# Optimization experiments

Measured on AMD Instinct MI355X. Metric: run time of the kernel, lower is better.

Reference implementation:

```python
import jax, jax.numpy as jnp
import numpy as np
from jax import lax

B, CO, CI, KH, KW, H, W = 32, 128, 128, 3, 3, 56, 56
STRIDE = (1, 1)
PADDING = ((1, 1), (1, 1))


def setup_inputs() -> dict:
    key = jax.random.key(0)
    k1, k2, k3, k4 = jax.random.split(key, 4)
    inp = jax.random.normal(k1, (B, CI, H, W), dtype=jnp.float32)
    eps = jax.random.normal(k2, (B, CO, CI, KH, KW), dtype=jnp.float32)
    # reset_parameters: psi ~ U(-6, -5); mu ~ U(-stdv, stdv), stdv = 1/sqrt(CI*KH*KW)
    weight_psi = jax.random.uniform(k3, (CO, CI, KH, KW), dtype=jnp.float32,
                                    minval=-6.0, maxval=-5.0)
    stdv = 1.0 / np.sqrt(CI * KH * KW)
    weight_mu = jax.random.uniform(k4, (CO, CI, KH, KW), dtype=jnp.float32,
                                   minval=-stdv, maxval=stdv)
    return {"input": inp, "eps": eps, "weight_psi": weight_psi, "weight_mu": weight_mu}


def reference(input, eps, weight_psi, weight_mu):
    # mul_exp_add: per-sample weight = eps * exp(psi) + mu  -> [B, CO, CI, KH, KW]
    weight = eps * jnp.exp(weight_psi) + weight_mu

    # Per-example conv (torch does it via groups = bs trick); here vmap over batch.
    def conv_one(x, w):  # x: [CI,H,W], w: [CO,CI,KH,KW]
        return lax.conv_general_dilated(
            x[None], w, window_strides=STRIDE, padding=PADDING,
            dimension_numbers=("NCHW", "OIHW", "NCHW"))[0]

    out = jax.vmap(conv_one)(input, weight)  # [B, CO, H, W]
    return out
```

## Files before the change

### kernel.cpp

```cpp
#include <hip/hip_runtime.h>
#include <hip/hip_bf16.h>

#define CO    128
#define CI    128
#define NPIX  3136
#define PH    58
#define PPIX  3364
#define HPX   232
#define SROW  272

typedef __bf16 bf16x8 __attribute__((ext_vector_type(8)));
typedef float  f32x4  __attribute__((ext_vector_type(4)));

__global__ void prep_all(const float* __restrict__ in,
                         const float* __restrict__ eps,
                         const float* __restrict__ psi,
                         const float* __restrict__ mu,
                         __bf16* __restrict__ wt,
                         __bf16* __restrict__ it) {
  __shared__ __align__(16) __bf16 T[64][136];
  const int bx = blockIdx.x, tid = threadIdx.x;

  if (bx < 2048) {
    int idx = bx * 256 + tid;
    int ci = idx & 127;
    int co = (idx >> 7) & 127;
    const float* e  = eps + (size_t)idx * 9;
    const float* ps = psi + (size_t)(co * CI + ci) * 9;
    const float* m  = mu  + (size_t)(co * CI + ci) * 9;
    float v[9];
#pragma unroll
    for (int p = 0; p < 9; ++p) v[p] = e[p] * __expf(ps[p]) + m[p];
    int b = idx >> 14;
    __bf16* w = wt + ((size_t)b * 9 * CO + co) * CI + ci;
#pragma unroll
    for (int p = 0; p < 9; ++p) w[(size_t)p * CO * CI] = (__bf16)v[p];
  } else if (bx < 2504) {
    int cid = (bx - 2048) * 256 + tid;
    int pid = cid >> 4;
    int chunk = cid & 15;
    int b = pid / 228;
    int e = pid - b * 228;
    int ph, pw;
    if (e < 58)       { ph = 0;       pw = e; }
    else if (e < 116) { ph = 57;      pw = e - 58; }
    else if (e < 172) { ph = e - 115; pw = 0; }
    else              { ph = e - 171; pw = 57; }
    f32x4 z = {0.f, 0.f, 0.f, 0.f};
    *(f32x4*)&it[((size_t)b * PPIX + ph * PH + pw) * CI + chunk * 8] = z;
  } else {
    int tx = bx - 2504;
    int b  = tx / 49;
    int p0 = (tx - b * 49) * 64;
    const float* src = in + (size_t)b * CI * NPIX;
#pragma unroll
    for (int jj = 0; jj < 8; ++jj) {
      int c = jj * 256 + tid;
      int ci = c >> 4, xc = c & 15;
      float4 v = *(const float4*)(src + (size_t)ci * NPIX + p0 + xc * 4);
      T[xc * 4 + 0][ci] = (__bf16)v.x;
      T[xc * 4 + 1][ci] = (__bf16)v.y;
      T[xc * 4 + 2][ci] = (__bf16)v.z;
      T[xc * 4 + 3][ci] = (__bf16)v.w;
    }
    __syncthreads();
    __bf16* dstb = it + (size_t)b * PPIX * CI;
#pragma unroll
    for (int jj = 0; jj < 4; ++jj) {
      int c = jj * 256 + tid;
      int pl = c >> 4, xc = c & 15;
      int pix = p0 + pl;
      int oh = pix / 56, ow = pix - oh * 56;
      int ppix = (oh + 1) * PH + (ow + 1);
      *(f32x4*)&dstb[(size_t)ppix * CI + xc * 8] = *(const f32x4*)&T[pl][xc * 8];
    }
  }
}

__device__ __forceinline__ void loadB(const char* Bsh, const int* bbase, int tapb,
                                      bf16x8 bf[7]) {
#pragma unroll
  for (int nf = 0; nf < 7; ++nf)
    bf[nf] = *(const bf16x8*)&Bsh[bbase[nf] + tapb];
}

__device__ __forceinline__ void loadA(const __bf16* wtb, const int* ab, int s,
                                      bf16x8 af[4]) {
  const int p   = s >> 2;
  const int ci0 = (s & 3) << 5;
  const __bf16* ap = wtb + p * (CO * CI) + ci0;
#pragma unroll
  for (int mf = 0; mf < 4; ++mf)
    af[mf] = *(const bf16x8*)(ap + ab[mf]);
}

__device__ __forceinline__ void do_mfma(const bf16x8 af[4], const bf16x8 bf[7],
                                        f32x4 acc[4][7]) {
#pragma unroll
  for (int mf = 0; mf < 4; ++mf)
#pragma unroll
    for (int nf = 0; nf < 7; ++nf)
      acc[mf][nf] = __builtin_amdgcn_mfma_f32_16x16x32_bf16(
          af[mf], bf[nf], acc[mf][nf], 0, 0, 0);
}

#define TAPB(s) ((((s) >> 2) / 3) * PH + (((s) >> 2) % 3)) * SROW + (((s) & 3) << 6)

__global__ __launch_bounds__(128, 1) void bconv_gemm(
    const __bf16* __restrict__ wt,
    const __bf16* __restrict__ it,
    float* __restrict__ out) {
  __shared__ __align__(16) char Bsh[HPX * SROW];
  const int tid  = threadIdx.x;
  const int w    = tid >> 6;
  const int lane = tid & 63;
  const int quad = lane >> 4;
  const int l15  = lane & 15;

  const int lin = blockIdx.x;
  const int x   = lin & 7;
  const int j   = lin >> 3;
  const int bhi = j & 3;
  const int tile = j >> 2;
  const int b   = x + 8 * bhi;
  const int oh0 = tile * 2;

  const __bf16* hsrc = it + ((size_t)b * PPIX + oh0 * PH) * CI;
#pragma unroll
  for (int i = 0; i < 29; ++i) {
    int idx = i * 128 + tid;
    int px = idx >> 4, sub = idx & 15;
    f32x4 v = *(const f32x4*)(hsrc + (size_t)idx * 8);
    *(f32x4*)&Bsh[px * SROW + sub * 16] = v;
  }
  __syncthreads();

  int bbase[7];
#pragma unroll
  for (int nf = 0; nf < 7; ++nf) {
    int n = nf * 16 + l15;
    int r = (n >= 56) ? 1 : 0;
    bbase[nf] = (n + 2 * r) * SROW + quad * 16;
  }

  const int co0 = w * 64;
  const __bf16* wtb = wt + (size_t)b * 9 * CO * CI;
  int ab[4];
#pragma unroll
  for (int mf = 0; mf < 4; ++mf)
    ab[mf] = (co0 + mf * 16 + l15) * CI + quad * 8;

  f32x4 acc[4][7] = {};
  bf16x8 a0[4], a1[4], b0[7], b1[7];

  loadA(wtb, ab, 0, a0);
  loadB(Bsh, bbase, TAPB(0), b0);
#pragma unroll
  for (int s = 0; s < 34; s += 2) {
    loadA(wtb, ab, s + 1, a1);
    loadB(Bsh, bbase, TAPB(s + 1), b1);
    do_mfma(a0, b0, acc);
    loadA(wtb, ab, s + 2, a0);
    loadB(Bsh, bbase, TAPB(s + 2), b0);
    do_mfma(a1, b1, acc);
  }
  loadA(wtb, ab, 35, a1);
  loadB(Bsh, bbase, TAPB(35), b1);
  do_mfma(a0, b0, acc);
  do_mfma(a1, b1, acc);

  float* ob = out + (size_t)b * CO * NPIX + oh0 * 56;
#pragma unroll
  for (int mf = 0; mf < 4; ++mf) {
#pragma unroll
    for (int nf = 0; nf < 7; ++nf) {
#pragma unroll
      for (int r = 0; r < 4; ++r) {
        int co = co0 + mf * 16 + quad * 4 + r;
        ob[(size_t)co * NPIX + nf * 16 + l15] = acc[mf][nf][r];
      }
    }
  }
}

extern "C" void kernel_launch(void* const* d_in, const int* in_sizes, int n_in,
                              void* d_out, int out_size, void* d_ws, size_t ws_size,
                              hipStream_t stream) {
  const float* inp = (const float*)d_in[0];
  const float* eps = (const float*)d_in[1];
  const float* psi = (const float*)d_in[2];
  const float* mu  = (const float*)d_in[3];

  __bf16* wt = (__bf16*)d_ws;
  __bf16* it = (__bf16*)((char*)d_ws + 9437184);

  prep_all<<<4072, 256, 0, stream>>>(inp, eps, psi, mu, wt, it);
  bconv_gemm<<<896, 128, 0, stream>>>(wt, it, (float*)d_out);
}
```

Measured before the change: 166.7 us.

## Load conv input tile directly from global memory instead of staging in LDS

Removes the shared-memory staging of the padded input halo (about 63 KB) and its barrier in the GEMM kernel. B fragments are now read straight from the bf16 NHWC input in global memory, relying on L1/L2 for reuse across taps. Launch bounds are raised to allow two blocks per CU now that LDS use is zero. The trade-off is more global/cache traffic per MFMA, with B fetches taking global-load latency instead of LDS latency.

```diff
diff --git a/kernel.cpp b/kernel.cpp
--- a/kernel.cpp
+++ b/kernel.cpp
@@ -6,8 +6,6 @@
 #define NPIX  3136
 #define PH    58
 #define PPIX  3364
-#define HPX   232
-#define SROW  272
 
 typedef __bf16 bf16x8 __attribute__((ext_vector_type(8)));
 typedef float  f32x4  __attribute__((ext_vector_type(4)));
@@ -77,13 +75,6 @@
   }
 }
 
-__device__ __forceinline__ void loadB(const char* Bsh, const int* bbase, int tapb,
-                                      bf16x8 bf[7]) {
-#pragma unroll
-  for (int nf = 0; nf < 7; ++nf)
-    bf[nf] = *(const bf16x8*)&Bsh[bbase[nf] + tapb];
-}
-
 __device__ __forceinline__ void loadA(const __bf16* wtb, const int* ab, int s,
                                       bf16x8 af[4]) {
   const int p   = s >> 2;
@@ -92,6 +83,17 @@
 #pragma unroll
   for (int mf = 0; mf < 4; ++mf)
     af[mf] = *(const bf16x8*)(ap + ab[mf]);
+}
+
+__device__ __forceinline__ void loadB(const __bf16* itb, const int* br, int s,
+                                      bf16x8 bf[7]) {
+  const int p   = s >> 2;
+  const int ci0 = (s & 3) << 5;
+  const int kh  = p / 3, kw = p - kh * 3;
+  const int off = (kh * PH + kw - (PH + 1)) * CI + ci0;
+#pragma unroll
+  for (int nf = 0; nf < 7; ++nf)
+    bf[nf] = *(const bf16x8*)(itb + br[nf] + off);
 }
 
 __device__ __forceinline__ void do_mfma(const bf16x8 af[4], const bf16x8 bf[7],
@@ -104,13 +106,10 @@
           af[mf], bf[nf], acc[mf][nf], 0, 0, 0);
 }
 
-#define TAPB(s) ((((s) >> 2) / 3) * PH + (((s) >> 2) % 3)) * SROW + (((s) & 3) << 6)
-
-__global__ __launch_bounds__(128, 1) void bconv_gemm(
+__global__ __launch_bounds__(128, 2) void bconv_gemm(
     const __bf16* __restrict__ wt,
     const __bf16* __restrict__ it,
     float* __restrict__ out) {
-  __shared__ __align__(16) char Bsh[HPX * SROW];
   const int tid  = threadIdx.x;
   const int w    = tid >> 6;
   const int lane = tid & 63;
@@ -125,47 +124,40 @@
   const int b   = x + 8 * bhi;
   const int oh0 = tile * 2;
 
-  const __bf16* hsrc = it + ((size_t)b * PPIX + oh0 * PH) * CI;
-#pragma unroll
-  for (int i = 0; i < 29; ++i) {
-    int idx = i * 128 + tid;
-    int px = idx >> 4, sub = idx & 15;
-    f32x4 v = *(const f32x4*)(hsrc + (size_t)idx * 8);
-    *(f32x4*)&Bsh[px * SROW + sub * 16] = v;
-  }
-  __syncthreads();
-
-  int bbase[7];
-#pragma unroll
-  for (int nf = 0; nf < 7; ++nf) {
-    int n = nf * 16 + l15;
-    int r = (n >= 56) ? 1 : 0;
-    bbase[nf] = (n + 2 * r) * SROW + quad * 16;
-  }
+  const __bf16* wtb = wt + (size_t)b * 9 * CO * CI;
+  const __bf16* itb = it + (size_t)b * PPIX * CI;
 
   const int co0 = w * 64;
-  const __bf16* wtb = wt + (size_t)b * 9 * CO * CI;
   int ab[4];
 #pragma unroll
   for (int mf = 0; mf < 4; ++mf)
     ab[mf] = (co0 + mf * 16 + l15) * CI + quad * 8;
 
+  int br[7];
+#pragma unroll
+  for (int nf = 0; nf < 7; ++nf) {
+    int n = nf * 16 + l15;
+    int r = (n >= 56) ? 1 : 0;
+    int c = n - r * 56;
+    br[nf] = ((oh0 + 1 + r) * PH + (c + 1)) * CI + quad * 8;
+  }
+
   f32x4 acc[4][7] = {};
   bf16x8 a0[4], a1[4], b0[7], b1[7];
 
   loadA(wtb, ab, 0, a0);
-  loadB(Bsh, bbase, TAPB(0), b0);
+  loadB(itb, br, 0, b0);
 #pragma unroll
   for (int s = 0; s < 34; s += 2) {
     loadA(wtb, ab, s + 1, a1);
-    loadB(Bsh, bbase, TAPB(s + 1), b1);
+    loadB(itb, br, s + 1, b1);
     do_mfma(a0, b0, acc);
     loadA(wtb, ab, s + 2, a0);
-    loadB(Bsh, bbase, TAPB(s + 2), b0);
+    loadB(itb, br, s + 2, b0);
     do_mfma(a1, b1, acc);
   }
   loadA(wtb, ab, 35, a1);
-  loadB(Bsh, bbase, TAPB(35), b1);
+  loadB(itb, br, 35, b1);
   do_mfma(a0, b0, acc);
   do_mfma(a1, b1, acc);
 
```

Result: slower. 207.7 us (+24.6%).
